# Optimization experiments

Hardware: AMD Instinct MI355X
Metric: run time of the kernel (lower is better)

The kernel has to match this reference:

```python
import jax, jax.numpy as jnp
import numpy as np

TAU = 1.0
NUM_CLASSES = 14
LOSS_WEIGHT = 1.0


def setup_inputs() -> dict:
    key = jax.random.key(0)
    k1, k2, k3 = jax.random.split(key, 3)
    B, C, H, W = 8, NUM_CLASSES, 512, 512
    preds_S = jax.random.normal(k1, (B, C, H, W), dtype=jnp.float32)
    preds_T = jax.random.normal(k2, (B, C, H, W), dtype=jnp.float32)
    gt_labels = jax.random.randint(k3, (B, 1, H, W), 0, NUM_CLASSES, dtype=jnp.int32)
    return {"preds_S": preds_S, "preds_T": preds_T, "gt_labels": gt_labels}


def _boundaries(gt):
    # gt: [B, H, W] int. Per-class binary mask for classes 1..NUM_CLASSES-1,
    # boundary = mask XOR binary_erosion(mask) with cross (connectivity-1)
    # structuring element and zero border (scipy/cupy ndimage default).
    classes = jnp.arange(1, NUM_CLASSES, dtype=gt.dtype)  # [K]
    m = gt[:, None, :, :] == classes[None, :, None, None]  # [B, K, H, W] bool
    mp = jnp.pad(m, ((0, 0), (0, 0), (1, 1), (1, 1)))  # zero border
    eroded = (m
              & mp[:, :, :-2, 1:-1]   # up
              & mp[:, :, 2:, 1:-1]    # down
              & mp[:, :, 1:-1, :-2]   # left
              & mp[:, :, 1:-1, 2:])   # right
    return m ^ eroded  # [B, K, H, W] bool


def reference(preds_S, preds_T, gt_labels):
    B, C, H, W = preds_S.shape
    P = H * W
    dt = preds_S.dtype

    boundary = _boundaries(gt_labels[:, 0]).reshape(B, NUM_CLASSES - 1, P)
    bf = boundary.astype(dt)  # [B, K, P]

    # Channel-dim (dim=0 of the [C, HW] view) softmax is per-pixel, so
    # gathering boundary pixels then softmaxing == softmax everywhere + mask.
    log_pS = jax.nn.log_softmax(preds_S / TAU, axis=1).reshape(B, C, P)
    log_pT = jax.nn.log_softmax(preds_T / TAU, axis=1).reshape(B, C, P)
    pT = jnp.exp(log_pT)
    # pointwise KL summed over channels, per pixel: [B, P]
    kl_pix = jnp.sum(pT * (log_pT - log_pS), axis=1)

    n = jnp.sum(bf, axis=-1)                              # [B, K] boundary sizes
    kl_sum = jnp.einsum('bkp,bp->bk', bf, kl_pix)         # [B, K]
    # Original skips when idxs.sum() == 0, i.e. sum of flat boundary indices
    # is zero (no boundary pixels, or sole boundary pixel at index 0).
    idx = jnp.arange(P, dtype=dt)
    idx_sum = jnp.einsum('bkp,p->bk', bf, idx)            # [B, K]
    valid = idx_sum > 0
    # F.kl_div reduction='mean' divides by total elements = C * n
    terms = jnp.where(valid, kl_sum / (C * jnp.maximum(n, 1.0)), 0.0)
    loss = LOSS_WEIGHT * (TAU ** 2) * jnp.sum(terms)
    return loss
```

## Files before the change

kernel.cpp:

```cpp
#include <hip/hip_runtime.h>


#define CC 14
#define KB 13
#define BB 8
#define HH 512
#define WW 512
#define PP (HH * WW)
#define PIX_PER_BLOCK 1024
#define BLOCKS_PER_IMG (PP / PIX_PER_BLOCK)

#define NBINS (BB * KB)

__device__ __forceinline__ float4 f4max(float4 a, float4 b) {
    return make_float4(fmaxf(a.x, b.x), fmaxf(a.y, b.y), fmaxf(a.z, b.z), fmaxf(a.w, b.w));
}
__device__ __forceinline__ float4 f4sub(float4 a, float4 b) {
    return make_float4(a.x - b.x, a.y - b.y, a.z - b.z, a.w - b.w);
}
__device__ __forceinline__ float4 f4exp(float4 a) {
    return make_float4(__expf(a.x), __expf(a.y), __expf(a.z), __expf(a.w));
}

__global__ void zero_ws_kernel(float* __restrict__ ws) {
    int i = threadIdx.x;
    if (i < 2 * NBINS) ws[i] = 0.0f;
}

__global__ __launch_bounds__(256, 1) void boundary_kl_kernel(
        const float* __restrict__ S, const float* __restrict__ T,
        const int* __restrict__ gt, float* __restrict__ ws) {
    const int tid = threadIdx.x;
    const int b   = blockIdx.x / BLOCKS_PER_IMG;
    const int p0  = (blockIdx.x % BLOCKS_PER_IMG) * PIX_PER_BLOCK + tid * 4;

    __shared__ float s_kl[KB + 1];
    __shared__ float s_n[KB + 1];
    if (tid <= KB) { s_kl[tid] = 0.0f; s_n[tid] = 0.0f; }
    __syncthreads();

    const float* Sb = S + (size_t)b * CC * PP + p0;
    const float* Tb = T + (size_t)b * CC * PP + p0;
    const int*  gtb = gt + (size_t)b * PP;

    float4 xs[CC], xt[CC];
#pragma unroll
    for (int c = 0; c < CC; ++c) xs[c] = *(const float4*)(Sb + (size_t)c * PP);
#pragma unroll
    for (int c = 0; c < CC; ++c) xt[c] = *(const float4*)(Tb + (size_t)c * PP);

    const int h = p0 >> 9;
    const int w = p0 & (WW - 1);
    int4 g = *(const int4*)(gtb + p0);
    int4 gu = make_int4(-1, -1, -1, -1);
    int4 gd = make_int4(-1, -1, -1, -1);
    if (h > 0)      gu = *(const int4*)(gtb + p0 - WW);
    if (h < HH - 1) gd = *(const int4*)(gtb + p0 + WW);
    const int gl = (w > 0)       ? gtb[p0 - 1] : -1;
    const int gr = (w + 4 < WW)  ? gtb[p0 + 4] : -1;

    asm volatile("" ::: "memory");

    float4 mS = xs[0], mT = xt[0];
#pragma unroll
    for (int c = 1; c < CC; ++c) { mS = f4max(mS, xs[c]); mT = f4max(mT, xt[c]); }

    float4 zS = make_float4(0.f, 0.f, 0.f, 0.f);
    float4 zT = make_float4(0.f, 0.f, 0.f, 0.f);
    float4 A  = make_float4(0.f, 0.f, 0.f, 0.f);
#pragma unroll
    for (int c = 0; c < CC; ++c) {
        float4 eS = f4exp(f4sub(xs[c], mS));
        float4 eT = f4exp(f4sub(xt[c], mT));
        zS.x += eS.x; zS.y += eS.y; zS.z += eS.z; zS.w += eS.w;
        zT.x += eT.x; zT.y += eT.y; zT.z += eT.z; zT.w += eT.w;
        float4 d = f4sub(xt[c], xs[c]);
        A.x += eT.x * d.x; A.y += eT.y * d.y; A.z += eT.z * d.z; A.w += eT.w * d.w;
    }
    float kl[4];
    kl[0] = A.x / zT.x + (mS.x + __logf(zS.x)) - (mT.x + __logf(zT.x));
    kl[1] = A.y / zT.y + (mS.y + __logf(zS.y)) - (mT.y + __logf(zT.y));
    kl[2] = A.z / zT.z + (mS.z + __logf(zS.z)) - (mT.z + __logf(zT.z));
    kl[3] = A.w / zT.w + (mS.w + __logf(zS.w)) - (mT.w + __logf(zT.w));

    const int gc[4]  = {g.x, g.y, g.z, g.w};
    const int gup[4] = {gu.x, gu.y, gu.z, gu.w};
    const int gdn[4] = {gd.x, gd.y, gd.z, gd.w};
    const int glf[4] = {gl, g.x, g.y, g.z};
    const int grt[4] = {g.y, g.z, g.w, gr};

#pragma unroll
    for (int j = 0; j < 4; ++j) {
        const int k = gc[j];
        const bool eroded = (glf[j] == k) & (grt[j] == k) & (gup[j] == k) & (gdn[j] == k);
        if (k >= 1 && !eroded) {
            atomicAdd(&s_kl[k], kl[j]);
            atomicAdd(&s_n[k], 1.0f);
        }
    }
    __syncthreads();

    if (tid >= 1 && tid <= KB) {
        atomicAdd(&ws[b * KB + (tid - 1)], s_kl[tid]);
        atomicAdd(&ws[NBINS + b * KB + (tid - 1)], s_n[tid]);
    }
}

__global__ void finalize_kernel(const float* __restrict__ ws,
                                const int* __restrict__ gt,
                                float* __restrict__ out) {
    __shared__ float partial[128];
    const int tid = threadIdx.x;
    float t = 0.0f;
    if (tid < NBINS) {
        const int b = tid / KB;
        const int k = (tid % KB) + 1;
        const float kl = ws[tid];
        const float n  = ws[NBINS + tid];
        const int k0 = gt[(size_t)b * PP];
        const float sub = (k0 == k) ? 1.0f : 0.0f;
        const float npos = n - sub;
        t = (npos > 0.0f) ? (kl / ((float)CC * fmaxf(n, 1.0f))) : 0.0f;
    }
    partial[tid] = t;
    __syncthreads();
    for (int s = 64; s > 0; s >>= 1) {
        if (tid < s) partial[tid] += partial[tid + s];
        __syncthreads();
    }
    if (tid == 0) out[0] = partial[0];
}

extern "C" void kernel_launch(void* const* d_in, const int* in_sizes, int n_in,
                              void* d_out, int out_size, void* d_ws, size_t ws_size,
                              hipStream_t stream) {
    const float* S  = (const float*)d_in[0];
    const float* T  = (const float*)d_in[1];
    const int*   gt = (const int*)d_in[2];
    float* out = (float*)d_out;
    float* ws  = (float*)d_ws;

    hipLaunchKernelGGL(zero_ws_kernel, dim3(1), dim3(256), 0, stream, ws);
    hipLaunchKernelGGL(boundary_kl_kernel, dim3(BB * BLOCKS_PER_IMG), dim3(256), 0, stream,
                       S, T, gt, ws);
    hipLaunchKernelGGL(finalize_kernel, dim3(1), dim3(128), 0, stream, ws, gt, out);
}
```

Measured before the change: 254.6 us.

## Process 8 pixels per thread with streaming online softmax

```diff
diff --git a/kernel.cpp b/kernel.cpp
--- a/kernel.cpp
+++ b/kernel.cpp
@@ -7,32 +7,23 @@
 #define HH 512
 #define WW 512
 #define PP (HH * WW)
-#define PIX_PER_BLOCK 1024
-#define BLOCKS_PER_IMG (PP / PIX_PER_BLOCK)
+#define PXT 8
+#define PXB (256 * PXT)
+#define BLOCKS_PER_IMG (PP / PXB)
 
 #define NBINS (BB * KB)
-
-__device__ __forceinline__ float4 f4max(float4 a, float4 b) {
-    return make_float4(fmaxf(a.x, b.x), fmaxf(a.y, b.y), fmaxf(a.z, b.z), fmaxf(a.w, b.w));
-}
-__device__ __forceinline__ float4 f4sub(float4 a, float4 b) {
-    return make_float4(a.x - b.x, a.y - b.y, a.z - b.z, a.w - b.w);
-}
-__device__ __forceinline__ float4 f4exp(float4 a) {
-    return make_float4(__expf(a.x), __expf(a.y), __expf(a.z), __expf(a.w));
-}
 
 __global__ void zero_ws_kernel(float* __restrict__ ws) {
     int i = threadIdx.x;
     if (i < 2 * NBINS) ws[i] = 0.0f;
 }
 
-__global__ __launch_bounds__(256, 1) void boundary_kl_kernel(
+__global__ __launch_bounds__(256, 3) void boundary_kl_kernel(
         const float* __restrict__ S, const float* __restrict__ T,
         const int* __restrict__ gt, float* __restrict__ ws) {
     const int tid = threadIdx.x;
     const int b   = blockIdx.x / BLOCKS_PER_IMG;
-    const int p0  = (blockIdx.x % BLOCKS_PER_IMG) * PIX_PER_BLOCK + tid * 4;
+    const int p0  = (blockIdx.x % BLOCKS_PER_IMG) * PXB;
 
     __shared__ float s_kl[KB + 1];
     __shared__ float s_n[KB + 1];
@@ -43,59 +34,76 @@
     const float* Tb = T + (size_t)b * CC * PP + p0;
     const int*  gtb = gt + (size_t)b * PP;
 
-    float4 xs[CC], xt[CC];
+    const int o0 = 4 * tid;
+    const int o1 = 1024 + 4 * tid;
+
+    int contrib_mask = 0;
+    int kcls[PXT];
 #pragma unroll
-    for (int c = 0; c < CC; ++c) xs[c] = *(const float4*)(Sb + (size_t)c * PP);
+    for (int half = 0; half < 2; ++half) {
+        const int pbase = p0 + (half ? o1 : o0);
+        const int h = pbase >> 9;
+        const int w = pbase & (WW - 1);
+        int4 g  = *(const int4*)(gtb + pbase);
+        int4 gu = make_int4(-1, -1, -1, -1);
+        int4 gd = make_int4(-1, -1, -1, -1);
+        if (h > 0)      gu = *(const int4*)(gtb + pbase - WW);
+        if (h < HH - 1) gd = *(const int4*)(gtb + pbase + WW);
+        const int gl = (w > 0)      ? gtb[pbase - 1] : -1;
+        const int gr = (w + 4 < WW) ? gtb[pbase + 4] : -1;
+        const int gc[4]  = {g.x, g.y, g.z, g.w};
+        const int gup[4] = {gu.x, gu.y, gu.z, gu.w};
+        const int gdn[4] = {gd.x, gd.y, gd.z, gd.w};
+        const int glf[4] = {gl, g.x, g.y, g.z};
+        const int grt[4] = {g.y, g.z, g.w, gr};
 #pragma unroll
-    for (int c = 0; c < CC; ++c) xt[c] = *(const float4*)(Tb + (size_t)c * PP);
+        for (int j = 0; j < 4; ++j) {
+            const int i = half * 4 + j;
+            const int k = gc[j];
+            kcls[i] = k;
+            const bool eroded = (glf[j] == k) & (grt[j] == k) & (gup[j] == k) & (gdn[j] == k);
+            if (k >= 1 && !eroded) contrib_mask |= (1 << i);
+        }
+    }
 
-    const int h = p0 >> 9;
-    const int w = p0 & (WW - 1);
-    int4 g = *(const int4*)(gtb + p0);
-    int4 gu = make_int4(-1, -1, -1, -1);
-    int4 gd = make_int4(-1, -1, -1, -1);
-    if (h > 0)      gu = *(const int4*)(gtb + p0 - WW);
-    if (h < HH - 1) gd = *(const int4*)(gtb + p0 + WW);
-    const int gl = (w > 0)       ? gtb[p0 - 1] : -1;
-    const int gr = (w + 4 < WW)  ? gtb[p0 + 4] : -1;
+    float mS[PXT], mT[PXT], zS[PXT], zT[PXT], A[PXT];
+#pragma unroll
+    for (int i = 0; i < PXT; ++i) {
+        mS[i] = -1e30f; mT[i] = -1e30f;
+        zS[i] = 0.f; zT[i] = 0.f; A[i] = 0.f;
+    }
 
-    asm volatile("" ::: "memory");
-
-    float4 mS = xs[0], mT = xt[0];
-#pragma unroll
-    for (int c = 1; c < CC; ++c) { mS = f4max(mS, xs[c]); mT = f4max(mT, xt[c]); }
-
-    float4 zS = make_float4(0.f, 0.f, 0.f, 0.f);
-    float4 zT = make_float4(0.f, 0.f, 0.f, 0.f);
-    float4 A  = make_float4(0.f, 0.f, 0.f, 0.f);
 #pragma unroll
     for (int c = 0; c < CC; ++c) {
-        float4 eS = f4exp(f4sub(xs[c], mS));
-        float4 eT = f4exp(f4sub(xt[c], mT));
-        zS.x += eS.x; zS.y += eS.y; zS.z += eS.z; zS.w += eS.w;
-        zT.x += eT.x; zT.y += eT.y; zT.z += eT.z; zT.w += eT.w;
-        float4 d = f4sub(xt[c], xs[c]);
-        A.x += eT.x * d.x; A.y += eT.y * d.y; A.z += eT.z * d.z; A.w += eT.w * d.w;
+        const float* Sc = Sb + (size_t)c * PP;
+        const float* Tc = Tb + (size_t)c * PP;
+        const float4 sA = *(const float4*)(Sc + o0);
+        const float4 sB = *(const float4*)(Sc + o1);
+        const float4 tA = *(const float4*)(Tc + o0);
+        const float4 tB = *(const float4*)(Tc + o1);
+        const float xs[PXT] = {sA.x, sA.y, sA.z, sA.w, sB.x, sB.y, sB.z, sB.w};
+        const float xt[PXT] = {tA.x, tA.y, tA.z, tA.w, tB.x, tB.y, tB.z, tB.w};
+#pragma unroll
+        for (int i = 0; i < PXT; ++i) {
+            const float nmS = fmaxf(mS[i], xs[i]);
+            zS[i] = zS[i] * __expf(mS[i] - nmS) + __expf(xs[i] - nmS);
+            mS[i] = nmS;
+            const float nmT = fmaxf(mT[i], xt[i]);
+            const float sc = __expf(mT[i] - nmT);
+            const float e  = __expf(xt[i] - nmT);
+            zT[i] = zT[i] * sc + e;
+            A[i]  = A[i]  * sc + e * (xt[i] - xs[i]);
+            mT[i] = nmT;
+        }
     }
-    float kl[4];
-    kl[0] = A.x / zT.x + (mS.x + __logf(zS.x)) - (mT.x + __logf(zT.x));
-    kl[1] = A.y / zT.y + (mS.y + __logf(zS.y)) - (mT.y + __logf(zT.y));
-    kl[2] = A.z / zT.z + (mS.z + __logf(zS.z)) - (mT.z + __logf(zT.z));
-    kl[3] = A.w / zT.w + (mS.w + __logf(zS.w)) - (mT.w + __logf(zT.w));
-
-    const int gc[4]  = {g.x, g.y, g.z, g.w};
-    const int gup[4] = {gu.x, gu.y, gu.z, gu.w};
-    const int gdn[4] = {gd.x, gd.y, gd.z, gd.w};
-    const int glf[4] = {gl, g.x, g.y, g.z};
-    const int grt[4] = {g.y, g.z, g.w, gr};
 
 #pragma unroll
-    for (int j = 0; j < 4; ++j) {
-        const int k = gc[j];
-        const bool eroded = (glf[j] == k) & (grt[j] == k) & (gup[j] == k) & (gdn[j] == k);
-        if (k >= 1 && !eroded) {
-            atomicAdd(&s_kl[k], kl[j]);
-            atomicAdd(&s_n[k], 1.0f);
+    for (int i = 0; i < PXT; ++i) {
+        if (contrib_mask & (1 << i)) {
+            const float kl = A[i] / zT[i] + (mS[i] + __logf(zS[i]))
+                                         - (mT[i] + __logf(zT[i]));
+            atomicAdd(&s_kl[kcls[i]], kl);
+            atomicAdd(&s_n[kcls[i]], 1.0f);
         }
     }
     __syncthreads();
```

New measurement: 358.3 us. 40.7% more time.
